# Kernel optimization log

Measured on AMD Instinct MI355X. Metric: run time of the kernel, lower is better.

Reference implementation:

```python
import jax, jax.numpy as jnp
import numpy as np
from math import sqrt

B, N, CS, H, D, K = 8, 256, 512, 8, 64, 32
NB = 2 * K + 1          # no_bins = 65
CT = 2048               # c_transition
INF = 1e9
WL = sqrt(0.5)          # w_L
EPS = 1e-5


def setup_inputs() -> dict:
    key = jax.random.key(0)
    ks = jax.random.split(key, 10)
    sc = 0.02
    return {
        "s": jax.random.normal(ks[0], (B, N, CS), jnp.float32),
        "masks": jnp.ones((B, N), jnp.bool_),
        "wq": jax.random.normal(ks[1], (CS, D * H), jnp.float32) * sc,
        "wk": jax.random.normal(ks[2], (CS, D * H), jnp.float32) * sc,
        "wv": jax.random.normal(ks[3], (CS, D * H), jnp.float32) * sc,
        "wb": jax.random.normal(ks[4], (NB, H), jnp.float32) * sc,
        "wo": jax.random.normal(ks[5], ((NB + D) * H, CS), jnp.float32) * sc,
        "bo": jnp.zeros((CS,), jnp.float32),
        "ln1_g": jnp.ones((CS,), jnp.float32),
        "ln1_b": jnp.zeros((CS,), jnp.float32),
        "w1": jax.random.normal(ks[6], (CS, CT), jnp.float32) * sc,
        "b1": jnp.zeros((CT,), jnp.float32),
        "w2": jax.random.normal(ks[7], (CT, CS), jnp.float32) * sc,
        "b2": jnp.zeros((CS,), jnp.float32),
        "ln2_g": jnp.ones((CS,), jnp.float32),
        "ln2_b": jnp.zeros((CS,), jnp.float32),
    }


def _layernorm(x, g, b):
    m = jnp.mean(x, -1, keepdims=True)
    v = jnp.var(x, -1, keepdims=True)
    return (x - m) * jax.lax.rsqrt(v + EPS) * g + b


def _heads(x):  # [B,N,D*H] -> [B,H,N,D]  (torch: reshape(B,N,D,H) then move H forward)
    return jnp.transpose(x.reshape(B, N, D, H), (0, 3, 1, 2))


def reference(s, masks, wq, wk, wv, wb, wo, bo, ln1_g, ln1_b, w1, b1, w2, b2, ln2_g, ln2_b):
    mf = masks.astype(s.dtype)                       # [B,N]
    sq = mf[:, :, None] * mf[:, None, :]             # [B,N,N]

    # relative position one-hot, clipped to [-K, K] -> [N,N,NB]
    r = jnp.arange(N)
    dmat = jnp.clip(r[:, None] - r[None, :], -K, K) + K
    relpos_base = jax.nn.one_hot(dmat, NB, dtype=s.dtype)
    relpos = relpos_base[None] * sq[..., None]       # [B,N,N,NB]

    b_bias = jnp.einsum('bijc,ch->bhij', relpos, wb)  # [B,H,N,N]

    q = _heads(s @ wq)                               # [B,H,N,D]
    k = _heads(s @ wk)
    v = _heads(s @ wv)

    logits = WL * (jnp.einsum('bhid,bhjd->bhij', q, k) / sqrt(D) + b_bias)
    logits = logits - INF * (1.0 - sq)[:, None]      # mask
    a = jax.nn.softmax(logits, axis=-1)              # [B,H,N,N]

    # pairwise aggregation and value aggregation (einsum avoids [B,H,N,N,NB] blowup)
    o_pair = jnp.einsum('bhij,bijc->bhic', a, relpos)  # [B,H,N,NB]
    o = jnp.einsum('bhij,bhjd->bhid', a, v)            # [B,H,N,D]

    op = jnp.transpose(o_pair, (0, 2, 1, 3)).reshape(B, N, H * NB)
    ov = jnp.transpose(o, (0, 2, 1, 3)).reshape(B, N, H * D)
    embd = jnp.concatenate([op, ov], axis=-1) @ wo + bo   # [B,N,CS]

    x = _layernorm(s + embd, ln1_g, ln1_b)
    ff = jax.nn.relu(x @ w1 + b1) @ w2 + b2
    x = _layernorm(x + ff, ln2_g, ln2_b)
    return x, a
```

## Files before the change

kernel.cpp:

```cpp
#include <hip/hip_runtime.h>
#include <hip/hip_bf16.h>
#include <cstdint>

#define B_ 8
#define N_ 256
#define CS_ 512
#define H_ 8
#define D_ 64
#define K_ 32
#define NB_ 65
#define CT_ 2048
#define WL_ 0.70710678118654752f

typedef __attribute__((ext_vector_type(8))) short bf16x8;
typedef __attribute__((ext_vector_type(4))) float f32x4;

#define GLOBAL_AS __attribute__((address_space(1)))
#define LDS_AS __attribute__((address_space(3)))

__device__ __forceinline__ void async16(void* lds, const void* g) {
  __builtin_amdgcn_global_load_lds((const GLOBAL_AS uint32_t*)g,
                                   (LDS_AS uint32_t*)lds, 16, 0, 0);
}

__global__ __launch_bounds__(256) void gemm_bf16(
    const ushort* __restrict__ A, const ushort* __restrict__ Bt,
    const float* __restrict__ bias, float* __restrict__ C,
    ushort* __restrict__ Cb, int M, int Nc, int Kd, int flags) {
  __shared__ ushort As[128 * 64];
  __shared__ ushort Bs[128 * 64];
  int tid = threadIdx.x;
  int bm = blockIdx.y * 128, bn = blockIdx.x * 128;
  int S = gridDim.z, z = blockIdx.z;
  int T = Kd >> 6;
  int it0 = (z * T) / S, it1 = ((z + 1) * T) / S;
  if (flags & 8) C += (size_t)z * M * Nc;
  int w = tid >> 6, l = tid & 63;
  int wr = (w >> 1) * 64, wc = (w & 1) * 64;
  int lm = l & 15, lq = l >> 4;
  int srow = tid >> 3;
  int sg = tid & 7;

  f32x4 acc[4][4];
#pragma unroll
  for (int i = 0; i < 4; ++i)
#pragma unroll
    for (int j = 0; j < 4; ++j) acc[i][j] = (f32x4){0.f, 0.f, 0.f, 0.f};

  for (int it = it0; it < it1; ++it) {
    int k0 = it << 6;
    __syncthreads();
#pragma unroll
    for (int r = 0; r < 4; ++r) {
      int row = r * 32 + srow;
      int gl = sg ^ (row & 7);
      async16(&As[row * 64 + sg * 8],
              A + (size_t)(bm + row) * Kd + k0 + gl * 8);
      async16(&Bs[row * 64 + sg * 8],
              Bt + (size_t)(bn + row) * Kd + k0 + gl * 8);
    }
    __syncthreads();
#pragma unroll
    for (int kk = 0; kk < 2; ++kk) {
      bf16x8 af[4], bfr[4];
#pragma unroll
      for (int i = 0; i < 4; ++i) {
        int ma = wr + 16 * i + lm;
        af[i] = *(const bf16x8*)&As[ma * 64 + ((kk * 4 + lq) ^ (ma & 7)) * 8];
        int nb = wc + 16 * i + lm;
        bfr[i] = *(const bf16x8*)&Bs[nb * 64 + ((kk * 4 + lq) ^ (nb & 7)) * 8];
      }
#pragma unroll
      for (int i = 0; i < 4; ++i)
#pragma unroll
        for (int j = 0; j < 4; ++j)
          acc[i][j] = __builtin_amdgcn_mfma_f32_16x16x32_bf16(
              af[i], bfr[j], acc[i][j], 0, 0, 0);
    }
  }
#pragma unroll
  for (int j = 0; j < 4; ++j) {
    int col = bn + wc + 16 * j + lm;
    float bv = ((flags & 1) && z == 0) ? bias[col] : 0.f;
#pragma unroll
    for (int i = 0; i < 4; ++i) {
#pragma unroll
      for (int r = 0; r < 4; ++r) {
        int row = bm + wr + 16 * i + lq * 4 + r;
        float v = acc[i][j][r] + bv;
        if (flags & 2) v = fmaxf(v, 0.f);
        if (flags & 8) C[(size_t)row * Nc + col] = v;
        if (flags & 4) {
          __hip_bfloat16 hb = __float2bfloat16(v);
          Cb[(size_t)row * Nc + col] = *(ushort*)&hb;
        }
        if (flags & 16) {
          int which = col >> 9, c = col & 511;
          int hh = c >> 6, d2 = c & 63;
          int bb = row >> 8, nn = row & 255;
          __hip_bfloat16 hb = __float2bfloat16(v);
          size_t dst;
          if (which == 2)
            dst = (size_t)2 * 1048576 + (((size_t)(bb * 8 + hh) * 64) + d2) * 256 + nn;
          else
            dst = (size_t)which * 1048576 + (((size_t)(bb * 8 + hh) * 256) + nn) * 64 + d2;
          Cb[dst] = *(ushort*)&hb;
        }
      }
    }
  }
}

__global__ __launch_bounds__(256) void transpose_all(
    const float* __restrict__ wq, const float* __restrict__ wk,
    const float* __restrict__ wv, const float* __restrict__ wo,
    const float* __restrict__ w1, const float* __restrict__ w2,
    __hip_bfloat16* __restrict__ wqkvT, __hip_bfloat16* __restrict__ wopT,
    __hip_bfloat16* __restrict__ w1T, __hip_bfloat16* __restrict__ w2T) {
  __shared__ float tile[32][33];
  int blk = blockIdx.x;
  const float* src;
  __hip_bfloat16* dst;
  int R, C, Kpad, tX, tIdx, whichBase = -1;
  if (blk < 768) {
    int zz = blk >> 8; tIdx = blk & 255;
    src = zz == 0 ? wq : zz == 1 ? wk : wv;
    dst = wqkvT; whichBase = zz * 512; R = 512; C = 512; Kpad = 512; tX = 16;
  } else if (blk < 1312) {
    tIdx = blk - 768; src = wo; dst = wopT; R = 1032; C = 512; Kpad = 1088; tX = 16;
  } else if (blk < 2336) {
    tIdx = blk - 1312; src = w1; dst = w1T; R = 512; C = 2048; Kpad = 512; tX = 64;
  } else {
    tIdx = blk - 2336; src = w2; dst = w2T; R = 2048; C = 512; Kpad = 2048; tX = 16;
  }
  int c0 = (tIdx % tX) * 32, r0 = (tIdx / tX) * 32;
  int tx = threadIdx.x & 31, ty = threadIdx.x >> 5;
#pragma unroll
  for (int yy = 0; yy < 32; yy += 8) {
    int r = r0 + ty + yy, c = c0 + tx;
    tile[ty + yy][tx] = (r < R && c < C) ? src[(size_t)r * C + c] : 0.f;
  }
  __syncthreads();
#pragma unroll
  for (int yy = 0; yy < 32; yy += 8) {
    int cc = c0 + ty + yy, k = r0 + tx;
    if (cc < C && k < Kpad) {
      int n = (whichBase >= 0) ? (whichBase + (cc & 7) * 64 + (cc >> 3)) : cc;
      dst[(size_t)n * Kpad + k] = __float2bfloat16(tile[tx][ty + yy]);
    }
  }
}

__global__ void cvt_bf16(const float* __restrict__ src,
                         __hip_bfloat16* __restrict__ dst, int n4) {
  int i = blockIdx.x * 256 + threadIdx.x;
  if (i >= n4) return;
  float4 v = ((const float4*)src)[i];
  dst[i * 4 + 0] = __float2bfloat16(v.x);
  dst[i * 4 + 1] = __float2bfloat16(v.y);
  dst[i * 4 + 2] = __float2bfloat16(v.z);
  dst[i * 4 + 3] = __float2bfloat16(v.w);
}

__global__ __launch_bounds__(256) void attn_mfma(
    const ushort* __restrict__ qh, const ushort* __restrict__ kh,
    const int* __restrict__ masks, const float* __restrict__ wb,
    float* __restrict__ a_out, ushort* __restrict__ a_bf,
    float* __restrict__ opair) {
  int strip = blockIdx.x & 3, bh = blockIdx.x >> 2;
  int h = bh & 7, b = bh >> 3;
  __shared__ ushort Ks[256 * 64];
  __shared__ ushort Qs[64 * 64];
  __shared__ float wbs[NB_];
  __shared__ float mfj[256];
  int tid = threadIdx.x;
  int srow = tid >> 3, sg = tid & 7;
#pragma unroll
  for (int rr = 0; rr < 8; ++rr) {
    int row = rr * 32 + srow;
    int gl = sg ^ (row & 7);
    async16(&Ks[row * 64 + sg * 8],
            kh + ((size_t)bh * 256 + row) * 64 + gl * 8);
  }
#pragma unroll
  for (int rr = 0; rr < 2; ++rr) {
    int row = rr * 32 + srow;
    int gl = sg ^ (row & 7);
    async16(&Qs[row * 64 + sg * 8],
            qh + ((size_t)bh * 256 + strip * 64 + row) * 64 + gl * 8);
  }
  if (tid < NB_) wbs[tid] = wb[tid * H_ + h];
  mfj[tid] = (masks[b * 256 + tid] != 0) ? 1.f : 0.f;
  __syncthreads();

  int w = tid >> 6, l = tid & 63, lm = l & 15, lq = l >> 4;
  bf16x8 qf[2];
#pragma unroll
  for (int kk = 0; kk < 2; ++kk) {
    int qrow = w * 16 + lm;
    qf[kk] = *(const bf16x8*)&Qs[qrow * 64 + ((kk * 4 + lq) ^ (qrow & 7)) * 8];
  }
  f32x4 acc[16];
#pragma unroll
  for (int ct = 0; ct < 16; ++ct) {
    int krow = ct * 16 + lm;
    bf16x8 kf0 = *(const bf16x8*)&Ks[krow * 64 + ((lq) ^ (krow & 7)) * 8];
    bf16x8 kf1 = *(const bf16x8*)&Ks[krow * 64 + ((4 + lq) ^ (krow & 7)) * 8];
    f32x4 zf = (f32x4){0.f, 0.f, 0.f, 0.f};
    zf = __builtin_amdgcn_mfma_f32_16x16x32_bf16(qf[0], kf0, zf, 0, 0, 0);
    acc[ct] = __builtin_amdgcn_mfma_f32_16x16x32_bf16(qf[1], kf1, acc[ct] = zf, 0, 0, 0);
  }
  int ibase = strip * 64 + w * 16 + lq * 4;
  float mfi[4];
#pragma unroll
  for (int r = 0; r < 4; ++r) mfi[r] = mfj[ibase + r];
#pragma unroll
  for (int ct = 0; ct < 16; ++ct) {
    int j = ct * 16 + lm;
    float mj = mfj[j];
#pragma unroll
    for (int r = 0; r < 4; ++r) {
      int i = ibase + r;
      int diff = i - j;
      int cb = diff < -K_ ? 0 : (diff > K_ ? 2 * K_ : diff + K_);
      float sq = mfi[r] * mj;
      acc[ct][r] = WL_ * (acc[ct][r] * 0.125f + wbs[cb] * sq) - 1e9f * (1.f - sq);
    }
  }
  float mx[4], sm[4];
#pragma unroll
  for (int r = 0; r < 4; ++r) {
    float m = acc[0][r];
#pragma unroll
    for (int ct = 1; ct < 16; ++ct) m = fmaxf(m, acc[ct][r]);
#pragma unroll
    for (int o = 1; o < 16; o <<= 1) m = fmaxf(m, __shfl_xor(m, o, 64));
    mx[r] = m;
  }
#pragma unroll
  for (int ct = 0; ct < 16; ++ct)
#pragma unroll
    for (int r = 0; r < 4; ++r) acc[ct][r] = __expf(acc[ct][r] - mx[r]);
#pragma unroll
  for (int r = 0; r < 4; ++r) {
    float s = 0.f;
#pragma unroll
    for (int ct = 0; ct < 16; ++ct) s += acc[ct][r];
#pragma unroll
    for (int o = 1; o < 16; o <<= 1) s += __shfl_xor(s, o, 64);
    sm[r] = 1.f / s;
  }
  float p0[4] = {0.f, 0.f, 0.f, 0.f}, p64[4] = {0.f, 0.f, 0.f, 0.f};
#pragma unroll
  for (int ct = 0; ct < 16; ++ct) {
    int j = ct * 16 + lm;
    float mj = mfj[j];
#pragma unroll
    for (int r = 0; r < 4; ++r) {
      int i = ibase + r;
      float aval = acc[ct][r] * sm[r];
      a_out[((size_t)bh * 256 + i) * 256 + j] = aval;
      __hip_bfloat16 hb = __float2bfloat16(aval);
      a_bf[((size_t)bh * 256 + i) * 256 + j] = *(ushort*)&hb;
      float val = aval * mfi[r] * mj;
      int diff = i - j;
      if (diff <= -K_)      p0[r] += val;
      else if (diff >= K_)  p64[r] += val;
      else opair[((size_t)bh * 256 + i) * NB_ + diff + K_] = val;
    }
  }
#pragma unroll
  for (int r = 0; r < 4; ++r)
#pragma unroll
    for (int o = 1; o < 16; o <<= 1) {
      p0[r]  += __shfl_xor(p0[r], o, 64);
      p64[r] += __shfl_xor(p64[r], o, 64);
    }
  if (lm == 0) {
#pragma unroll
    for (int r = 0; r < 4; ++r) {
      int i = ibase + r;
      opair[((size_t)bh * 256 + i) * NB_ + 0]      = p0[r];
      opair[((size_t)bh * 256 + i) * NB_ + 2 * K_] = p64[r];
    }
  }
#pragma unroll
  for (int r = 0; r < 4; ++r) {
    int i = ibase + r;
#pragma unroll
    for (int t = 0; t < 4; ++t) {
      int c = 1 + lm + 16 * t;
      if (c < 64) {
        int j = i - c + K_;
        if (j < 0 || j > 255)
          opair[((size_t)bh * 256 + i) * NB_ + c] = 0.f;
      }
    }
  }
}

__global__ __launch_bounds__(256) void av_mfma(
    const ushort* __restrict__ a_bf, const ushort* __restrict__ vT,
    float* __restrict__ o) {
  int bm = blockIdx.x * 128, bh = blockIdx.y;
  __shared__ ushort As[128 * 64];
  __shared__ ushort Bs[64 * 64];
  int tid = threadIdx.x;
  int w = tid >> 6, l = tid & 63, lm = l & 15, lq = l >> 4;
  int wr = (w >> 1) * 64, wc = (w & 1) * 32;
  int srow = tid >> 3, sg = tid & 7;
  const ushort* Abase = a_bf + (size_t)bh * 65536;
  const ushort* Bbase = vT + (size_t)bh * 16384;
  f32x4 acc[4][2];
#pragma unroll
  for (int i = 0; i < 4; ++i)
#pragma unroll
    for (int j = 0; j < 2; ++j) acc[i][j] = (f32x4){0.f, 0.f, 0.f, 0.f};
  for (int k0 = 0; k0 < 256; k0 += 64) {
    __syncthreads();
#pragma unroll
    for (int r = 0; r < 4; ++r) {
      int row = r * 32 + srow;
      int gl = sg ^ (row & 7);
      async16(&As[row * 64 + sg * 8],
              Abase + (size_t)(bm + row) * 256 + k0 + gl * 8);
    }
#pragma unroll
    for (int r = 0; r < 2; ++r) {
      int row = r * 32 + srow;
      int gl = sg ^ (row & 7);
      async16(&Bs[row * 64 + sg * 8],
              Bbase + (size_t)row * 256 + k0 + gl * 8);
    }
    __syncthreads();
#pragma unroll
    for (int kk = 0; kk < 2; ++kk) {
      bf16x8 af[4], bfr[2];
#pragma unroll
      for (int i = 0; i < 4; ++i) {
        int ma = wr + 16 * i + lm;
        af[i] = *(const bf16x8*)&As[ma * 64 + ((kk * 4 + lq) ^ (ma & 7)) * 8];
      }
#pragma unroll
      for (int j = 0; j < 2; ++j) {
        int nb = wc + 16 * j + lm;
        bfr[j] = *(const bf16x8*)&Bs[nb * 64 + ((kk * 4 + lq) ^ (nb & 7)) * 8];
      }
#pragma unroll
      for (int i = 0; i < 4; ++i)
#pragma unroll
        for (int j = 0; j < 2; ++j)
          acc[i][j] = __builtin_amdgcn_mfma_f32_16x16x32_bf16(
              af[i], bfr[j], acc[i][j], 0, 0, 0);
    }
  }
#pragma unroll
  for (int j = 0; j < 2; ++j) {
    int col = wc + 16 * j + lm;
#pragma unroll
    for (int i = 0; i < 4; ++i)
#pragma unroll
      for (int r = 0; r < 4; ++r) {
        int row = bm + wr + 16 * i + lq * 4 + r;
        o[((size_t)bh * 256 + row) * 64 + col] = acc[i][j][r];
      }
  }
}

__global__ void pack_cat(const float* __restrict__ opair,
                         const float* __restrict__ o,
                         __hip_bfloat16* __restrict__ cat) {
  int idx = blockIdx.x * 256 + threadIdx.x;
  if (idx >= 2048 * 1088) return;
  int m = idx / 1088, kk = idx - m * 1088;
  int b = m >> 8, n = m & 255;
  float v = 0.f;
  if (kk < 520) {
    int h = kk / 65, c = kk - h * 65;
    v = opair[(((size_t)(b * 8 + h) * 256) + n) * 65 + c];
  } else if (kk < 1032) {
    int k2 = kk - 520;
    int h = k2 >> 6, d = k2 & 63;
    v = o[(((size_t)(b * 8 + h) * 256) + n) * 64 + d];
  }
  cat[idx] = __float2bfloat16(v);
}

__device__ __forceinline__ float lnReduceSum(float v, float* red) {
#pragma unroll
  for (int o = 32; o > 0; o >>= 1) v += __shfl_xor(v, o, 64);
  int w = threadIdx.x >> 6;
  __syncthreads();
  if ((threadIdx.x & 63) == 0) red[w] = v;
  __syncthreads();
  return red[0] + red[1] + red[2] + red[3];
}

__global__ __launch_bounds__(256) void ln_sum(
    const float* __restrict__ x1, const float* __restrict__ xp,
    int S, int stride, const float* __restrict__ g,
    const float* __restrict__ bta, float* __restrict__ out,
    __hip_bfloat16* __restrict__ out_bf) {
  __shared__ float red[4];
  int row = blockIdx.x, tid = threadIdx.x;
  size_t base = (size_t)row * 512;
  float v0 = x1[base + tid];
  float v1 = x1[base + tid + 256];
  for (int s = 0; s < S; ++s) {
    v0 += xp[(size_t)s * stride + base + tid];
    v1 += xp[(size_t)s * stride + base + tid + 256];
  }
  float su = lnReduceSum(v0 + v1, red);
  float sq = lnReduceSum(v0 * v0 + v1 * v1, red);
  float mean = su * (1.f / 512.f);
  float var = sq * (1.f / 512.f) - mean * mean;
  float inv = rsqrtf(var + 1e-5f);
  float o0 = (v0 - mean) * inv * g[tid] + bta[tid];
  float o1 = (v1 - mean) * inv * g[tid + 256] + bta[tid + 256];
  out[base + tid]       = o0;
  out[base + tid + 256] = o1;
  if (out_bf) {
    out_bf[base + tid]       = __float2bfloat16(o0);
    out_bf[base + tid + 256] = __float2bfloat16(o1);
  }
}

extern "C" void kernel_launch(void* const* d_in, const int* in_sizes, int n_in,
                              void* d_out, int out_size, void* d_ws, size_t ws_size,
                              hipStream_t stream) {
  const float* s     = (const float*)d_in[0];
  const int*   masks = (const int*)d_in[1];
  const float* wq = (const float*)d_in[2];
  const float* wk = (const float*)d_in[3];
  const float* wv = (const float*)d_in[4];
  const float* wb = (const float*)d_in[5];
  const float* wo = (const float*)d_in[6];
  const float* bo = (const float*)d_in[7];
  const float* ln1_g = (const float*)d_in[8];
  const float* ln1_b = (const float*)d_in[9];
  const float* w1 = (const float*)d_in[10];
  const float* b1 = (const float*)d_in[11];
  const float* w2 = (const float*)d_in[12];
  const float* b2 = (const float*)d_in[13];
  const float* ln2_g = (const float*)d_in[14];
  const float* ln2_b = (const float*)d_in[15];

  float* out_x = (float*)d_out;
  float* out_a = out_x + 1048576;

  float* ws = (float*)d_ws;
  float* embd_part = ws + 0;
  float* xbuf      = ws + 4194304;
  float* ff_part   = ws + 5242880;
  float* obuf      = ws + 9437184;
  float* opair     = ws + 10485760;
  ushort* qkv_bf   = (ushort*)(ws + 11550720);
  ushort* q_bf = qkv_bf;
  ushort* k_bf = qkv_bf + 1048576;
  ushort* v_bf = qkv_bf + 2097152;
  ushort* a_bf     = (ushort*)(ws + 13123584);
  __hip_bfloat16* h_bf   = (__hip_bfloat16*)(ws + 15220736);
  __hip_bfloat16* s_bf   = (__hip_bfloat16*)(ws + 17317888);
  __hip_bfloat16* x_bf   = (__hip_bfloat16*)(ws + 17842176);
  __hip_bfloat16* cat_bf = (__hip_bfloat16*)(ws + 18366464);
  __hip_bfloat16* wqkvT  = (__hip_bfloat16*)(ws + 19480576);
  __hip_bfloat16* wopT   = (__hip_bfloat16*)(ws + 19873792);
  __hip_bfloat16* w1T    = (__hip_bfloat16*)(ws + 20152320);
  __hip_bfloat16* w2T    = (__hip_bfloat16*)(ws + 20676608);

  dim3 blk(256);
  cvt_bf16<<<dim3(1024), blk, 0, stream>>>(s, s_bf, 262144);
  transpose_all<<<dim3(3360), blk, 0, stream>>>(wq, wk, wv, wo, w1, w2,
                                                wqkvT, wopT, w1T, w2T);
  gemm_bf16<<<dim3(12, 16, 1), blk, 0, stream>>>(
      (const ushort*)s_bf, (const ushort*)wqkvT, nullptr, nullptr,
      qkv_bf, 2048, 1536, 512, 16);
  attn_mfma<<<dim3(256), blk, 0, stream>>>(q_bf, k_bf, masks, wb,
                                           out_a, a_bf, opair);
  av_mfma<<<dim3(2, 64), blk, 0, stream>>>(a_bf, v_bf, obuf);
  pack_cat<<<dim3(8704), blk, 0, stream>>>(opair, obuf, cat_bf);
  gemm_bf16<<<dim3(4, 16, 4), blk, 0, stream>>>(
      (const ushort*)cat_bf, (const ushort*)wopT, bo, embd_part, nullptr,
      2048, 512, 1088, 1 | 8);
  ln_sum<<<dim3(2048), blk, 0, stream>>>(s, embd_part, 4, 1048576,
                                         ln1_g, ln1_b, xbuf, x_bf);
  gemm_bf16<<<dim3(16, 16, 1), blk, 0, stream>>>(
      (const ushort*)x_bf, (const ushort*)w1T, b1, nullptr, (ushort*)h_bf,
      2048, 2048, 512, 1 | 2 | 4);
  gemm_bf16<<<dim3(4, 16, 4), blk, 0, stream>>>(
      (const ushort*)h_bf, (const ushort*)w2T, b2, ff_part, nullptr,
      2048, 512, 2048, 1 | 8);
  ln_sum<<<dim3(2048), blk, 0, stream>>>(xbuf, ff_part, 4, 1048576,
                                         ln2_g, ln2_b, out_x, nullptr);
}
```

Baseline: 207.2 us.

## Fuse attention, AV product and concat packing; merge input conversion into weight prep

The attention kernel now computes the P·V product itself, staging bf16 probabilities and V tiles in reused LDS. It writes the pair and value outputs straight into the bf16 concat buffer, so the separate av_mfma and pack_cat kernels go away along with the fp32 opair/obuf and bf16 attention intermediates. The s-to-bf16 conversion is folded into the weight-transpose kernel, which drops one more launch. In exchange the attention kernel takes on more work and more synchronisation per block, and it only has 256 blocks of parallelism for the AV stage.

```diff
diff --git a/kernel.cpp b/kernel.cpp
--- a/kernel.cpp
+++ b/kernel.cpp
@@ -21,6 +21,11 @@
 __device__ __forceinline__ void async16(void* lds, const void* g) {
   __builtin_amdgcn_global_load_lds((const GLOBAL_AS uint32_t*)g,
                                    (LDS_AS uint32_t*)lds, 16, 0, 0);
+}
+
+__device__ __forceinline__ ushort f2bf(float v) {
+  __hip_bfloat16 hb = __float2bfloat16(v);
+  return *(ushort*)&hb;
 }
 
 __global__ __launch_bounds__(256) void gemm_bf16(
@@ -90,35 +95,42 @@
         float v = acc[i][j][r] + bv;
         if (flags & 2) v = fmaxf(v, 0.f);
         if (flags & 8) C[(size_t)row * Nc + col] = v;
-        if (flags & 4) {
-          __hip_bfloat16 hb = __float2bfloat16(v);
-          Cb[(size_t)row * Nc + col] = *(ushort*)&hb;
-        }
+        if (flags & 4) Cb[(size_t)row * Nc + col] = f2bf(v);
         if (flags & 16) {
           int which = col >> 9, c = col & 511;
           int hh = c >> 6, d2 = c & 63;
           int bb = row >> 8, nn = row & 255;
-          __hip_bfloat16 hb = __float2bfloat16(v);
           size_t dst;
           if (which == 2)
             dst = (size_t)2 * 1048576 + (((size_t)(bb * 8 + hh) * 64) + d2) * 256 + nn;
           else
             dst = (size_t)which * 1048576 + (((size_t)(bb * 8 + hh) * 256) + nn) * 64 + d2;
-          Cb[dst] = *(ushort*)&hb;
+          Cb[dst] = f2bf(v);
         }
       }
     }
   }
 }
 
-__global__ __launch_bounds__(256) void transpose_all(
+__global__ __launch_bounds__(256) void prep_all(
+    const float* __restrict__ s, __hip_bfloat16* __restrict__ s_bf,
     const float* __restrict__ wq, const float* __restrict__ wk,
     const float* __restrict__ wv, const float* __restrict__ wo,
     const float* __restrict__ w1, const float* __restrict__ w2,
     __hip_bfloat16* __restrict__ wqkvT, __hip_bfloat16* __restrict__ wopT,
     __hip_bfloat16* __restrict__ w1T, __hip_bfloat16* __restrict__ w2T) {
+  int blk = blockIdx.x;
+  if (blk < 1024) {
+    int i = blk * 256 + threadIdx.x;
+    float4 v = ((const float4*)s)[i];
+    s_bf[i * 4 + 0] = __float2bfloat16(v.x);
+    s_bf[i * 4 + 1] = __float2bfloat16(v.y);
+    s_bf[i * 4 + 2] = __float2bfloat16(v.z);
+    s_bf[i * 4 + 3] = __float2bfloat16(v.w);
+    return;
+  }
+  blk -= 1024;
   __shared__ float tile[32][33];
-  int blk = blockIdx.x;
   const float* src;
   __hip_bfloat16* dst;
   int R, C, Kpad, tX, tIdx, whichBase = -1;
@@ -151,28 +163,20 @@
   }
 }
 
-__global__ void cvt_bf16(const float* __restrict__ src,
-                         __hip_bfloat16* __restrict__ dst, int n4) {
-  int i = blockIdx.x * 256 + threadIdx.x;
-  if (i >= n4) return;
-  float4 v = ((const float4*)src)[i];
-  dst[i * 4 + 0] = __float2bfloat16(v.x);
-  dst[i * 4 + 1] = __float2bfloat16(v.y);
-  dst[i * 4 + 2] = __float2bfloat16(v.z);
-  dst[i * 4 + 3] = __float2bfloat16(v.w);
-}
-
-__global__ __launch_bounds__(256) void attn_mfma(
+__global__ __launch_bounds__(256) void attn_fused(
     const ushort* __restrict__ qh, const ushort* __restrict__ kh,
-    const int* __restrict__ masks, const float* __restrict__ wb,
-    float* __restrict__ a_out, ushort* __restrict__ a_bf,
-    float* __restrict__ opair) {
+    const ushort* __restrict__ vT, const int* __restrict__ masks,
+    const float* __restrict__ wb, float* __restrict__ a_out,
+    ushort* __restrict__ cat) {
   int strip = blockIdx.x & 3, bh = blockIdx.x >> 2;
   int h = bh & 7, b = bh >> 3;
-  __shared__ ushort Ks[256 * 64];
-  __shared__ ushort Qs[64 * 64];
+  __shared__ ushort lds[20480];
   __shared__ float wbs[NB_];
   __shared__ float mfj[256];
+  ushort* Ks = lds;
+  ushort* Qs = lds + 16384;
+  ushort* Vh = lds;
+  ushort* Ps = lds + 8192;
   int tid = threadIdx.x;
   int srow = tid >> 3, sg = tid & 7;
 #pragma unroll
@@ -208,7 +212,7 @@
     bf16x8 kf1 = *(const bf16x8*)&Ks[krow * 64 + ((4 + lq) ^ (krow & 7)) * 8];
     f32x4 zf = (f32x4){0.f, 0.f, 0.f, 0.f};
     zf = __builtin_amdgcn_mfma_f32_16x16x32_bf16(qf[0], kf0, zf, 0, 0, 0);
-    acc[ct] = __builtin_amdgcn_mfma_f32_16x16x32_bf16(qf[1], kf1, acc[ct] = zf, 0, 0, 0);
+    acc[ct] = __builtin_amdgcn_mfma_f32_16x16x32_bf16(qf[1], kf1, zf, 0, 0, 0);
   }
   int ibase = strip * 64 + w * 16 + lq * 4;
   float mfi[4];
@@ -260,13 +264,11 @@
       int i = ibase + r;
       float aval = acc[ct][r] * sm[r];
       a_out[((size_t)bh * 256 + i) * 256 + j] = aval;
-      __hip_bfloat16 hb = __float2bfloat16(aval);
-      a_bf[((size_t)bh * 256 + i) * 256 + j] = *(ushort*)&hb;
       float val = aval * mfi[r] * mj;
       int diff = i - j;
       if (diff <= -K_)      p0[r] += val;
       else if (diff >= K_)  p64[r] += val;
-      else opair[((size_t)bh * 256 + i) * NB_ + diff + K_] = val;
+      else cat[((size_t)(b * 256 + i)) * 1088 + h * 65 + diff + K_] = f2bf(val);
     }
   }
 #pragma unroll
@@ -280,8 +282,8 @@
 #pragma unroll
     for (int r = 0; r < 4; ++r) {
       int i = ibase + r;
-      opair[((size_t)bh * 256 + i) * NB_ + 0]      = p0[r];
-      opair[((size_t)bh * 256 + i) * NB_ + 2 * K_] = p64[r];
+      cat[((size_t)(b * 256 + i)) * 1088 + h * 65 + 0]      = f2bf(p0[r]);
+      cat[((size_t)(b * 256 + i)) * 1088 + h * 65 + 2 * K_] = f2bf(p64[r]);
     }
   }
 #pragma unroll
@@ -293,97 +295,65 @@
       if (c < 64) {
         int j = i - c + K_;
         if (j < 0 || j > 255)
-          opair[((size_t)bh * 256 + i) * NB_ + c] = 0.f;
+          cat[((size_t)(b * 256 + i)) * 1088 + h * 65 + c] = 0;
       }
     }
   }
-}
-
-__global__ __launch_bounds__(256) void av_mfma(
-    const ushort* __restrict__ a_bf, const ushort* __restrict__ vT,
-    float* __restrict__ o) {
-  int bm = blockIdx.x * 128, bh = blockIdx.y;
-  __shared__ ushort As[128 * 64];
-  __shared__ ushort Bs[64 * 64];
-  int tid = threadIdx.x;
-  int w = tid >> 6, l = tid & 63, lm = l & 15, lq = l >> 4;
-  int wr = (w >> 1) * 64, wc = (w & 1) * 32;
-  int srow = tid >> 3, sg = tid & 7;
-  const ushort* Abase = a_bf + (size_t)bh * 65536;
-  const ushort* Bbase = vT + (size_t)bh * 16384;
-  f32x4 acc[4][2];
-#pragma unroll
-  for (int i = 0; i < 4; ++i)
-#pragma unroll
-    for (int j = 0; j < 2; ++j) acc[i][j] = (f32x4){0.f, 0.f, 0.f, 0.f};
-  for (int k0 = 0; k0 < 256; k0 += 64) {
+  if (h == 0) {
+    for (int idx = tid; idx < 64 * 56; idx += 256) {
+      int r = idx / 56, c = 1032 + idx - r * 56 * 1 - (idx / 56) * 0;
+      c = 1032 + (idx - r * 56);
+      cat[((size_t)(b * 256 + strip * 64 + r)) * 1088 + c] = 0;
+    }
+  }
+  __syncthreads();
+  f32x4 acc2[4];
+#pragma unroll
+  for (int nt = 0; nt < 4; ++nt) acc2[nt] = (f32x4){0.f, 0.f, 0.f, 0.f};
+  int vrow_ = tid >> 4, vsg = tid & 15;
+#pragma unroll
+  for (int hf = 0; hf < 2; ++hf) {
+    if (hf == 1) __syncthreads();
+#pragma unroll
+    for (int rr = 0; rr < 4; ++rr) {
+      int d = rr * 16 + vrow_;
+      int gl = vsg ^ (d & 7);
+      async16(&Vh[d * 128 + vsg * 8],
+              vT + (size_t)bh * 16384 + d * 256 + hf * 128 + gl * 8);
+    }
+#pragma unroll
+    for (int cl = 0; cl < 8; ++cl) {
+      int ct = hf * 8 + cl;
+#pragma unroll
+      for (int r = 0; r < 4; ++r) {
+        int rowl = w * 16 + lq * 4 + r;
+        float aval = acc[ct][r] * sm[r];
+        int g = cl * 2 + (lm >> 3);
+        Ps[rowl * 128 + ((g ^ (rowl & 7)) << 3) + (lm & 7)] = f2bf(aval);
+      }
+    }
     __syncthreads();
 #pragma unroll
+    for (int kst = 0; kst < 4; ++kst) {
+      int prow = w * 16 + lm;
+      bf16x8 af = *(const bf16x8*)&Ps[prow * 128 + (((kst * 4 + lq) ^ (prow & 7)) << 3)];
+#pragma unroll
+      for (int nt = 0; nt < 4; ++nt) {
+        int d = nt * 16 + lm;
+        bf16x8 bfr = *(const bf16x8*)&Vh[d * 128 + (((kst * 4 + lq) ^ (d & 7)) << 3)];
+        acc2[nt] = __builtin_amdgcn_mfma_f32_16x16x32_bf16(af, bfr, acc2[nt], 0, 0, 0);
+      }
+    }
+  }
+#pragma unroll
+  for (int nt = 0; nt < 4; ++nt) {
+    int d = nt * 16 + lm;
+#pragma unroll
     for (int r = 0; r < 4; ++r) {
-      int row = r * 32 + srow;
-      int gl = sg ^ (row & 7);
-      async16(&As[row * 64 + sg * 8],
-              Abase + (size_t)(bm + row) * 256 + k0 + gl * 8);
-    }
-#pragma unroll
-    for (int r = 0; r < 2; ++r) {
-      int row = r * 32 + srow;
-      int gl = sg ^ (row & 7);
-      async16(&Bs[row * 64 + sg * 8],
-              Bbase + (size_t)row * 256 + k0 + gl * 8);
-    }
-    __syncthreads();
-#pragma unroll
-    for (int kk = 0; kk < 2; ++kk) {
-      bf16x8 af[4], bfr[2];
-#pragma unroll
-      for (int i = 0; i < 4; ++i) {
-        int ma = wr + 16 * i + lm;
-        af[i] = *(const bf16x8*)&As[ma * 64 + ((kk * 4 + lq) ^ (ma & 7)) * 8];
-      }
-#pragma unroll
-      for (int j = 0; j < 2; ++j) {
-        int nb = wc + 16 * j + lm;
-        bfr[j] = *(const bf16x8*)&Bs[nb * 64 + ((kk * 4 + lq) ^ (nb & 7)) * 8];
-      }
-#pragma unroll
-      for (int i = 0; i < 4; ++i)
-#pragma unroll
-        for (int j = 0; j < 2; ++j)
-          acc[i][j] = __builtin_amdgcn_mfma_f32_16x16x32_bf16(
-              af[i], bfr[j], acc[i][j], 0, 0, 0);
-    }
-  }
-#pragma unroll
-  for (int j = 0; j < 2; ++j) {
-    int col = wc + 16 * j + lm;
-#pragma unroll
-    for (int i = 0; i < 4; ++i)
-#pragma unroll
-      for (int r = 0; r < 4; ++r) {
-        int row = bm + wr + 16 * i + lq * 4 + r;
-        o[((size_t)bh * 256 + row) * 64 + col] = acc[i][j][r];
-      }
-  }
-}
-
-__global__ void pack_cat(const float* __restrict__ opair,
-                         const float* __restrict__ o,
-                         __hip_bfloat16* __restrict__ cat) {
-  int idx = blockIdx.x * 256 + threadIdx.x;
-  if (idx >= 2048 * 1088) return;
-  int m = idx / 1088, kk = idx - m * 1088;
-  int b = m >> 8, n = m & 255;
-  float v = 0.f;
-  if (kk < 520) {
-    int h = kk / 65, c = kk - h * 65;
-    v = opair[(((size_t)(b * 8 + h) * 256) + n) * 65 + c];
-  } else if (kk < 1032) {
-    int k2 = kk - 520;
-    int h = k2 >> 6, d = k2 & 63;
-    v = o[(((size_t)(b * 8 + h) * 256) + n) * 64 + d];
-  }
-  cat[idx] = __float2bfloat16(v);
+      int i = ibase + r;
+      cat[((size_t)(b * 256 + i)) * 1088 + 520 + h * 64 + d] = f2bf(acc2[nt][r]);
+    }
+  }
 }
 
 __device__ __forceinline__ float lnReduceSum(float v, float* red) {
@@ -452,35 +422,29 @@
   float* embd_part = ws + 0;
   float* xbuf      = ws + 4194304;
   float* ff_part   = ws + 5242880;
-  float* obuf      = ws + 9437184;
-  float* opair     = ws + 10485760;
-  ushort* qkv_bf   = (ushort*)(ws + 11550720);
+  ushort* qkv_bf   = (ushort*)(ws + 9437184);
   ushort* q_bf = qkv_bf;
   ushort* k_bf = qkv_bf + 1048576;
   ushort* v_bf = qkv_bf + 2097152;
-  ushort* a_bf     = (ushort*)(ws + 13123584);
-  __hip_bfloat16* h_bf   = (__hip_bfloat16*)(ws + 15220736);
-  __hip_bfloat16* s_bf   = (__hip_bfloat16*)(ws + 17317888);
-  __hip_bfloat16* x_bf   = (__hip_bfloat16*)(ws + 17842176);
-  __hip_bfloat16* cat_bf = (__hip_bfloat16*)(ws + 18366464);
-  __hip_bfloat16* wqkvT  = (__hip_bfloat16*)(ws + 19480576);
-  __hip_bfloat16* wopT   = (__hip_bfloat16*)(ws + 19873792);
-  __hip_bfloat16* w1T    = (__hip_bfloat16*)(ws + 20152320);
-  __hip_bfloat16* w2T    = (__hip_bfloat16*)(ws + 20676608);
+  ushort* cat_bf = (ushort*)(ws + 10223616);
+  __hip_bfloat16* h_bf  = (__hip_bfloat16*)(ws + 11337728);
+  __hip_bfloat16* s_bf  = (__hip_bfloat16*)(ws + 13434880);
+  __hip_bfloat16* x_bf  = (__hip_bfloat16*)(ws + 13959168);
+  __hip_bfloat16* wqkvT = (__hip_bfloat16*)(ws + 14483456);
+  __hip_bfloat16* wopT  = (__hip_bfloat16*)(ws + 14876672);
+  __hip_bfloat16* w1T   = (__hip_bfloat16*)(ws + 15155200);
+  __hip_bfloat16* w2T   = (__hip_bfloat16*)(ws + 15679488);
 
   dim3 blk(256);
-  cvt_bf16<<<dim3(1024), blk, 0, stream>>>(s, s_bf, 262144);
-  transpose_all<<<dim3(3360), blk, 0, stream>>>(wq, wk, wv, wo, w1, w2,
-                                                wqkvT, wopT, w1T, w2T);
+  prep_all<<<dim3(4384), blk, 0, stream>>>(s, s_bf, wq, wk, wv, wo, w1, w2,
+                                           wqkvT, wopT, w1T, w2T);
   gemm_bf16<<<dim3(12, 16, 1), blk, 0, stream>>>(
       (const ushort*)s_bf, (const ushort*)wqkvT, nullptr, nullptr,
       qkv_bf, 2048, 1536, 512, 16);
-  attn_mfma<<<dim3(256), blk, 0, stream>>>(q_bf, k_bf, masks, wb,
-                                           out_a, a_bf, opair);
-  av_mfma<<<dim3(2, 64), blk, 0, stream>>>(a_bf, v_bf, obuf);
-  pack_cat<<<dim3(8704), blk, 0, stream>>>(opair, obuf, cat_bf);
+  attn_fused<<<dim3(256), blk, 0, stream>>>(q_bf, k_bf, v_bf, masks, wb,
+                                            out_a, cat_bf);
   gemm_bf16<<<dim3(4, 16, 4), blk, 0, stream>>>(
-      (const ushort*)cat_bf, (const ushort*)wopT, bo, embd_part, nullptr,
+      cat_bf, (const ushort*)wopT, bo, embd_part, nullptr,
       2048, 512, 1088, 1 | 8);
   ln_sum<<<dim3(2048), blk, 0, stream>>>(s, embd_part, 4, 1048576,
                                          ln1_g, ln1_b, xbuf, x_bf);
```

Result: faster. 197.1 us (-4.9%).
